# Kernel tuning notes

Hardware: AMD Instinct MI355X
Metric: run time of the kernel (lower is better)

The kernel has to match this reference:

```python
import jax, jax.numpy as jnp
from jax import lax
import numpy as np

B, T, D, H, K = 16, 1024, 1024, 1024, 2


def setup_inputs() -> dict:
    key = jax.random.key(0)
    k1, k2 = jax.random.split(key, 2)
    inputs = jax.random.normal(k1, (B, T, D), dtype=jnp.float32)
    # small init so tanh/sigmoid gates are not saturated
    conv_w = jax.random.normal(k2, (3 * H, D, K), dtype=jnp.float32) * 0.02
    conv_b = jnp.zeros((3 * H,), dtype=jnp.float32)
    return {"inputs": inputs, "conv_w": conv_w, "conv_b": conv_b, "layer_idx": 0}


def _qrnn_forward(inputs, conv_w, conv_b):
    k = conv_w.shape[-1]
    h = conv_w.shape[0] // 3
    # causal conv1d: pad (k-1) on the left of the time axis
    x = jnp.transpose(inputs, (0, 2, 1))                 # [B, D, T]
    x = jnp.pad(x, ((0, 0), (0, 0), (k - 1, 0)))         # [B, D, T+k-1]
    gates = lax.conv_general_dilated(
        x, conv_w, window_strides=(1,), padding="VALID",
        dimension_numbers=("NCH", "OIH", "NCH"))         # [B, 3H, T]
    gates = jnp.transpose(gates, (0, 2, 1)) + conv_b     # [B, T, 3H]
    Z = jnp.tanh(gates[..., :h])
    F = jax.nn.sigmoid(gates[..., h:2 * h])
    O = jax.nn.sigmoid(gates[..., 2 * h:])

    # fo-pooling recurrence: c_t = f_t * c_{t-1} + (1 - f_t) * z_t, c_0 = 0
    def step(c, zf):
        z, f = zf
        c_ = f * c + (1.0 - f) * z
        return c_, c_

    c0 = jnp.zeros((Z.shape[0], h), dtype=Z.dtype)
    zT = jnp.transpose(Z, (1, 0, 2))                     # [T, B, H]
    fT = jnp.transpose(F, (1, 0, 2))
    _, cT = lax.scan(step, c0, (zT, fT))                 # [T, B, H]
    c_time = jnp.transpose(cT, (1, 0, 2))                # [B, T, H]
    h_time = O * c_time
    return c_time, h_time


def reference(inputs, conv_w, conv_b, layer_idx):
    # layer_idx=0 with state=None, memory=None: no conv_linear memory term,
    # no attention, zero initial cell state.
    return _qrnn_forward(inputs, conv_w, conv_b)
```

## Files before the change

### kernel.cpp

```cpp
#include <hip/hip_runtime.h>

#define BB 16
#define TT 1024
#define DD 1024
#define HH 1024
#define NN 3072
#define KK 2048
#define MM (BB * TT)
#define TP (TT + 1)
#define NCH 32
#define TC  32

typedef __attribute__((ext_vector_type(8))) short short8;
typedef __attribute__((ext_vector_type(4))) float float4v;

__device__ __forceinline__ unsigned short f2bf(float f) {
    unsigned int u = __float_as_uint(f);
    u += 0x7fffu + ((u >> 16) & 1u);
    return (unsigned short)(u >> 16);
}
__device__ __forceinline__ float bf2f(unsigned short s) {
    return __uint_as_float(((unsigned int)s) << 16);
}

__device__ __forceinline__ void gload_lds16(const unsigned short* g, unsigned short* l) {
    __builtin_amdgcn_global_load_lds(
        (const __attribute__((address_space(1))) unsigned int*)(g),
        (__attribute__((address_space(3))) unsigned int*)(l),
        16, 0, 0);
}

__global__ __launch_bounds__(256) void pack_x_kernel(const float* __restrict__ x,
                                                     unsigned short* __restrict__ xpad) {
    int i = blockIdx.x * 256 + threadIdx.x;
    int total = BB * TP * (DD / 4);
    if (i >= total) return;
    int d4  = i & (DD / 4 - 1);
    int row = i >> 8;
    int b  = row / TP;
    int tp = row - b * TP;
    float4 v = make_float4(0.f, 0.f, 0.f, 0.f);
    if (tp > 0)
        v = ((const float4*)x)[(((size_t)(b * TT + tp - 1)) << 8) + d4];
    ushort4 r4;
    r4.x = f2bf(v.x); r4.y = f2bf(v.y); r4.z = f2bf(v.z); r4.w = f2bf(v.w);
    *(ushort4*)(xpad + (((size_t)row) << 10) + (d4 << 2)) = r4;
}

__global__ __launch_bounds__(256) void pack_w_kernel(const float* __restrict__ w,
                                                     unsigned short* __restrict__ Bt) {
    int i = blockIdx.x * 256 + threadIdx.x;
    if (i >= NN * DD) return;
    int n = i >> 10, d = i & 1023;
    float2 v = ((const float2*)w)[i];
    Bt[(size_t)n * KK + d]       = f2bf(v.x);
    Bt[(size_t)n * KK + DD + d]  = f2bf(v.y);
}

__global__ __launch_bounds__(256) void gemm_gates_kernel(const unsigned short* __restrict__ xpad,
                                                         const unsigned short* __restrict__ Bt,
                                                         const float* __restrict__ bias,
                                                         unsigned short* __restrict__ zfo) {
    __shared__ unsigned short As[128 * 32];
    __shared__ unsigned short Bs[128 * 32];

    const int tid  = threadIdx.x;
    const int lane = tid & 63;
    const int wave = tid >> 6;
    const int m0 = blockIdx.x * 128;
    const int n0 = blockIdx.y * 128;

    const int bidx = m0 >> 10;
    const int t0   = m0 & 1023;
    const unsigned short* aBase = xpad + (((size_t)(bidx * TP + t0)) << 10);

    const int msub = (wave & 1) << 6;
    const int nsub = (wave >> 1) << 6;
    const int mrow = lane & 15;
    const int quad = lane >> 4;
    const int csw = (quad ^ ((mrow >> 1) & 3)) << 3;

    float4v acc[4][4];
#pragma unroll
    for (int i = 0; i < 4; i++)
#pragma unroll
        for (int j = 0; j < 4; j++) acc[i][j] = (float4v)0.0f;

    for (int kb = 0; kb < KK / 32; ++kb) {
        const int tap = kb >> 5;
        const int kd0 = (kb & 31) << 5;
#pragma unroll
        for (int q = 0; q < 2; ++q) {
            int ci = q * 256 + tid;
            int r  = ci >> 2;
            int cs = (((ci & 3) ^ ((r >> 1) & 3)) << 3);
            gload_lds16(aBase + (((size_t)(r + tap)) << 10) + kd0 + cs, As + ci * 8);
            gload_lds16(Bt + (size_t)(n0 + r) * KK + (kb << 5) + cs, Bs + ci * 8);
        }
        __syncthreads();

        short8 af[4], bf[4];
#pragma unroll
        for (int i = 0; i < 4; i++) {
            af[i] = *(const short8*)(As + (msub + i * 16 + mrow) * 32 + csw);
            bf[i] = *(const short8*)(Bs + (nsub + i * 16 + mrow) * 32 + csw);
        }
#pragma unroll
        for (int i = 0; i < 4; i++)
#pragma unroll
            for (int j = 0; j < 4; j++)
                acc[i][j] = __builtin_amdgcn_mfma_f32_16x16x32_bf16(af[i], bf[j], acc[i][j], 0, 0, 0);
        __syncthreads();
    }

    const bool isZ = (n0 < HH);
#pragma unroll
    for (int j = 0; j < 4; j++) {
        int gcol = n0 + nsub + j * 16 + mrow;
        float bv = bias[gcol];
#pragma unroll
        for (int i = 0; i < 4; i++) {
            int mbase = m0 + msub + i * 16 + quad * 4;
#pragma unroll
            for (int r = 0; r < 4; r++) {
                float v = acc[i][j][r] + bv;
                float g;
                if (isZ) {
                    float s = __builtin_amdgcn_rcpf(1.0f + __expf(-2.0f * v));
                    g = 2.0f * s - 1.0f;
                } else {
                    g = __builtin_amdgcn_rcpf(1.0f + __expf(-v));
                }
                zfo[(size_t)(mbase + r) * NN + gcol] = f2bf(g);
            }
        }
    }
}


__global__ __launch_bounds__(256) void scan_summary_kernel(const unsigned short* __restrict__ zfo,
                                                           float2* __restrict__ P2,
                                                           float2* __restrict__ S2) {
    int g = blockIdx.x * 256 + threadIdx.x;
    int j = g >> 13;
    int b = (g >> 9) & 15;
    int h = (g & 511) << 1;
    const unsigned short* base = zfo + (size_t)b * TT * NN + h + (size_t)(j * TC) * NN;
    float c0 = 0.f, c1 = 0.f, p0 = 1.f, p1 = 1.f;
#pragma unroll 8
    for (int k = 0; k < TC; ++k) {
        const unsigned short* p = base + (size_t)k * NN;
        ushort2 z2 = *(const ushort2*)p;
        ushort2 f2 = *(const ushort2*)(p + HH);
        float z0 = bf2f(z2.x), z1 = bf2f(z2.y);
        float f0 = bf2f(f2.x), f1 = bf2f(f2.y);
        c0 = fmaf(f0, c0, (1.0f - f0) * z0);
        c1 = fmaf(f1, c1, (1.0f - f1) * z1);
        p0 *= f0;
        p1 *= f1;
    }
    P2[g] = make_float2(p0, p1);
    S2[g] = make_float2(c0, c1);
}

__global__ __launch_bounds__(256) void scan_prefix_kernel(const float* __restrict__ P,
                                                          const float* __restrict__ S,
                                                          float* __restrict__ Cin) {
    int idx = blockIdx.x * 256 + threadIdx.x;
    float c = 0.f;
#pragma unroll
    for (int j = 0; j < NCH; ++j) {
        int o = (j << 14) + idx;
        Cin[o] = c;
        c = fmaf(P[o], c, S[o]);
    }
}

__global__ __launch_bounds__(256) void scan_apply_kernel(const unsigned short* __restrict__ zfo,
                                                         const float2* __restrict__ Cin2,
                                                         float* __restrict__ out) {
    int g = blockIdx.x * 256 + threadIdx.x;
    int j = g >> 13;
    int b = (g >> 9) & 15;
    int h = (g & 511) << 1;
    const unsigned short* base = zfo + (size_t)b * TT * NN + h + (size_t)(j * TC) * NN;
    float* cp = out + (size_t)b * TT * HH + h + (size_t)(j * TC) * HH;
    float* hp = cp + (size_t)BB * TT * HH;
    float2 ci = Cin2[g];
    float c0 = ci.x, c1 = ci.y;
#pragma unroll 8
    for (int k = 0; k < TC; ++k) {
        const unsigned short* p = base + (size_t)k * NN;
        ushort2 z2 = *(const ushort2*)p;
        ushort2 f2 = *(const ushort2*)(p + HH);
        ushort2 o2 = *(const ushort2*)(p + 2 * HH);
        float z0 = bf2f(z2.x), z1 = bf2f(z2.y);
        float f0 = bf2f(f2.x), f1 = bf2f(f2.y);
        float o0 = bf2f(o2.x), o1 = bf2f(o2.y);
        c0 = fmaf(f0, c0, (1.0f - f0) * z0);
        c1 = fmaf(f1, c1, (1.0f - f1) * z1);
        *(float2*)(cp + (size_t)k * HH) = make_float2(c0, c1);
        *(float2*)(hp + (size_t)k * HH) = make_float2(o0 * c0, o1 * c1);
    }
}

extern "C" void kernel_launch(void* const* d_in, const int* in_sizes, int n_in,
                              void* d_out, int out_size, void* d_ws, size_t ws_size,
                              hipStream_t stream) {
    const float* x    = (const float*)d_in[0];
    const float* w    = (const float*)d_in[1];
    const float* bias = (const float*)d_in[2];
    float* out = (float*)d_out;

    char* ws = (char*)d_ws;
    const size_t xpad_bytes = (size_t)BB * TP * DD * 2;
    const size_t btw_bytes  = (size_t)NN * KK * 2;
    unsigned short* xpad = (unsigned short*)ws;
    unsigned short* Btw  = (unsigned short*)(ws + xpad_bytes);
    unsigned short* zfo  = (unsigned short*)(ws + xpad_bytes + btw_bytes);
    float* P   = (float*)ws;
    float* S   = (float*)(ws + (size_t)MM * NCH * 4);
    float* Cin = (float*)(ws + (size_t)MM * NCH * 8);

    {
        int total = BB * TP * (DD / 4);
        pack_x_kernel<<<(total + 255) / 256, 256, 0, stream>>>(x, xpad);
    }
    {
        int total = NN * DD;
        pack_w_kernel<<<(total + 255) / 256, 256, 0, stream>>>(w, Btw);
    }
    {
        dim3 grid(MM / 128, NN / 128);
        gemm_gates_kernel<<<grid, 256, 0, stream>>>(xpad, Btw, bias, zfo);
    }
    scan_summary_kernel<<<(MM / 2) * NCH / 256, 256, 0, stream>>>(zfo, (float2*)P, (float2*)S);
    scan_prefix_kernel<<<MM / 256, 256, 0, stream>>>(P, S, Cin);
    scan_apply_kernel<<<(MM / 2) * NCH / 256, 256, 0, stream>>>(zfo, (const float2*)Cin, out);
}
```

Before: 503.9 us.

## Store gate activations time-contiguous per gate plane via LDS transpose

The GEMM epilogue now stages activated gates in swizzled shared memory and writes them transposed into three separate planes (z, f, o), with time contiguous for each (batch, hidden) pair. The scan summary and apply kernels switch to one hidden unit per thread and read 32 timesteps with wide 16-byte vector loads instead of strided 4-byte loads. This targets the poorly coalesced reads in the scan phase. The trade-off is an extra LDS round trip and sync in the GEMM epilogue, and scan output stores become single floats strided by H across time.

```diff
diff --git a/kernel.cpp b/kernel.cpp
--- a/kernel.cpp
+++ b/kernel.cpp
@@ -10,6 +10,7 @@
 #define TP (TT + 1)
 #define NCH 32
 #define TC  32
+#define PLANE (1u << 24)
 
 typedef __attribute__((ext_vector_type(8))) short short8;
 typedef __attribute__((ext_vector_type(4))) float float4v;
@@ -60,9 +61,10 @@
 __global__ __launch_bounds__(256) void gemm_gates_kernel(const unsigned short* __restrict__ xpad,
                                                          const unsigned short* __restrict__ Bt,
                                                          const float* __restrict__ bias,
-                                                         unsigned short* __restrict__ zfo) {
-    __shared__ unsigned short As[128 * 32];
-    __shared__ unsigned short Bs[128 * 32];
+                                                         unsigned short* __restrict__ zT) {
+    __shared__ unsigned short smem[16384];
+    unsigned short* As = smem;
+    unsigned short* Bs = smem + 4096;
 
     const int tid  = threadIdx.x;
     const int lane = tid & 63;
@@ -112,55 +114,86 @@
                 acc[i][j] = __builtin_amdgcn_mfma_f32_16x16x32_bf16(af[i], bf[j], acc[i][j], 0, 0, 0);
         __syncthreads();
     }
+    unsigned short* Ts = smem;
 
     const bool isZ = (n0 < HH);
 #pragma unroll
     for (int j = 0; j < 4; j++) {
-        int gcol = n0 + nsub + j * 16 + mrow;
-        float bv = bias[gcol];
+        int nloc = nsub + j * 16 + mrow;
+        float bv = bias[n0 + nloc];
 #pragma unroll
         for (int i = 0; i < 4; i++) {
-            int mbase = m0 + msub + i * 16 + quad * 4;
-#pragma unroll
-            for (int r = 0; r < 4; r++) {
-                float v = acc[i][j][r] + bv;
-                float g;
+            int mcol = msub + i * 16 + (quad << 2);
+            unsigned int d0, d1;
+            {
+                float v0 = acc[i][j][0] + bv, v1 = acc[i][j][1] + bv;
+                float v2 = acc[i][j][2] + bv, v3 = acc[i][j][3] + bv;
+                float g0, g1, g2, g3;
                 if (isZ) {
-                    float s = __builtin_amdgcn_rcpf(1.0f + __expf(-2.0f * v));
-                    g = 2.0f * s - 1.0f;
+                    g0 = 2.0f * __builtin_amdgcn_rcpf(1.0f + __expf(-2.0f * v0)) - 1.0f;
+                    g1 = 2.0f * __builtin_amdgcn_rcpf(1.0f + __expf(-2.0f * v1)) - 1.0f;
+                    g2 = 2.0f * __builtin_amdgcn_rcpf(1.0f + __expf(-2.0f * v2)) - 1.0f;
+                    g3 = 2.0f * __builtin_amdgcn_rcpf(1.0f + __expf(-2.0f * v3)) - 1.0f;
                 } else {
-                    g = __builtin_amdgcn_rcpf(1.0f + __expf(-v));
+                    g0 = __builtin_amdgcn_rcpf(1.0f + __expf(-v0));
+                    g1 = __builtin_amdgcn_rcpf(1.0f + __expf(-v1));
+                    g2 = __builtin_amdgcn_rcpf(1.0f + __expf(-v2));
+                    g3 = __builtin_amdgcn_rcpf(1.0f + __expf(-v3));
                 }
-                zfo[(size_t)(mbase + r) * NN + gcol] = f2bf(g);
+                d0 = (unsigned int)f2bf(g0) | ((unsigned int)f2bf(g1) << 16);
+                d1 = (unsigned int)f2bf(g2) | ((unsigned int)f2bf(g3) << 16);
             }
-        }
-    }
-}
-
-
-__global__ __launch_bounds__(256) void scan_summary_kernel(const unsigned short* __restrict__ zfo,
-                                                           float2* __restrict__ P2,
-                                                           float2* __restrict__ S2) {
+            int chunk = (mcol >> 3) ^ (nloc & 7);
+            int el = nloc * 128 + (chunk << 3) + (mcol & 7);
+            *(uint2*)(Ts + el) = make_uint2(d0, d1);
+        }
+    }
+    __syncthreads();
+
+    const int rl = tid & 15;
+    const int rg = tid >> 4;
+    const int gate = n0 >> 10;
+    unsigned short* plane = zT + ((size_t)gate << 24);
+#pragma unroll
+    for (int p = 0; p < 8; p++) {
+        int np = (p << 4) + rg;
+        int lchunk = rl ^ (np & 7);
+        short8 vv = *(const short8*)(Ts + np * 128 + (lchunk << 3));
+        int h = (n0 & 1023) + np;
+        size_t dst = ((((size_t)((bidx << 10) | h)) << 10) | (unsigned)(t0 + (rl << 3)));
+        *(short8*)(plane + dst) = vv;
+    }
+}
+
+
+__global__ __launch_bounds__(256) void scan_summary_kernel(const unsigned short* __restrict__ zT,
+                                                           float* __restrict__ P,
+                                                           float* __restrict__ S) {
     int g = blockIdx.x * 256 + threadIdx.x;
-    int j = g >> 13;
-    int b = (g >> 9) & 15;
-    int h = (g & 511) << 1;
-    const unsigned short* base = zfo + (size_t)b * TT * NN + h + (size_t)(j * TC) * NN;
-    float c0 = 0.f, c1 = 0.f, p0 = 1.f, p1 = 1.f;
-#pragma unroll 8
-    for (int k = 0; k < TC; ++k) {
-        const unsigned short* p = base + (size_t)k * NN;
-        ushort2 z2 = *(const ushort2*)p;
-        ushort2 f2 = *(const ushort2*)(p + HH);
-        float z0 = bf2f(z2.x), z1 = bf2f(z2.y);
-        float f0 = bf2f(f2.x), f1 = bf2f(f2.y);
-        c0 = fmaf(f0, c0, (1.0f - f0) * z0);
-        c1 = fmaf(f1, c1, (1.0f - f1) * z1);
-        p0 *= f0;
-        p1 *= f1;
-    }
-    P2[g] = make_float2(p0, p1);
-    S2[g] = make_float2(c0, c1);
+    int h = g & 1023;
+    int b = (g >> 10) & 15;
+    int j = g >> 14;
+    const unsigned short* zp = zT + ((((size_t)((b << 10) | h)) << 10) + j * TC);
+    const unsigned short* fp = zp + PLANE;
+    short8 zv[4], fv[4];
+#pragma unroll
+    for (int q = 0; q < 4; ++q) {
+        zv[q] = *(const short8*)(zp + q * 8);
+        fv[q] = *(const short8*)(fp + q * 8);
+    }
+    float c = 0.f, pr = 1.f;
+#pragma unroll
+    for (int q = 0; q < 4; ++q)
+#pragma unroll
+        for (int k = 0; k < 8; ++k) {
+            float z = bf2f((unsigned short)zv[q][k]);
+            float f = bf2f((unsigned short)fv[q][k]);
+            c = fmaf(f, c, (1.0f - f) * z);
+            pr *= f;
+        }
+    int o = (j << 14) | (b << 10) | h;
+    P[o] = pr;
+    S[o] = c;
 }
 
 __global__ __launch_bounds__(256) void scan_prefix_kernel(const float* __restrict__ P,
@@ -176,32 +209,37 @@
     }
 }
 
-__global__ __launch_bounds__(256) void scan_apply_kernel(const unsigned short* __restrict__ zfo,
-                                                         const float2* __restrict__ Cin2,
+__global__ __launch_bounds__(256) void scan_apply_kernel(const unsigned short* __restrict__ zT,
+                                                         const float* __restrict__ Cin,
                                                          float* __restrict__ out) {
     int g = blockIdx.x * 256 + threadIdx.x;
-    int j = g >> 13;
-    int b = (g >> 9) & 15;
-    int h = (g & 511) << 1;
-    const unsigned short* base = zfo + (size_t)b * TT * NN + h + (size_t)(j * TC) * NN;
-    float* cp = out + (size_t)b * TT * HH + h + (size_t)(j * TC) * HH;
-    float* hp = cp + (size_t)BB * TT * HH;
-    float2 ci = Cin2[g];
-    float c0 = ci.x, c1 = ci.y;
-#pragma unroll 8
-    for (int k = 0; k < TC; ++k) {
-        const unsigned short* p = base + (size_t)k * NN;
-        ushort2 z2 = *(const ushort2*)p;
-        ushort2 f2 = *(const ushort2*)(p + HH);
-        ushort2 o2 = *(const ushort2*)(p + 2 * HH);
-        float z0 = bf2f(z2.x), z1 = bf2f(z2.y);
-        float f0 = bf2f(f2.x), f1 = bf2f(f2.y);
-        float o0 = bf2f(o2.x), o1 = bf2f(o2.y);
-        c0 = fmaf(f0, c0, (1.0f - f0) * z0);
-        c1 = fmaf(f1, c1, (1.0f - f1) * z1);
-        *(float2*)(cp + (size_t)k * HH) = make_float2(c0, c1);
-        *(float2*)(hp + (size_t)k * HH) = make_float2(o0 * c0, o1 * c1);
-    }
+    int h = g & 1023;
+    int b = (g >> 10) & 15;
+    int j = g >> 14;
+    const unsigned short* zp = zT + ((((size_t)((b << 10) | h)) << 10) + j * TC);
+    const unsigned short* fp = zp + PLANE;
+    const unsigned short* op = zp + 2 * (size_t)PLANE;
+    short8 zv[4], fv[4], ov[4];
+#pragma unroll
+    for (int q = 0; q < 4; ++q) {
+        zv[q] = *(const short8*)(zp + q * 8);
+        fv[q] = *(const short8*)(fp + q * 8);
+        ov[q] = *(const short8*)(op + q * 8);
+    }
+    float c = Cin[(j << 14) | (b << 10) | h];
+    float* cbase = out + ((((size_t)((b << 10) | (j * TC))) << 10) | h);
+#pragma unroll
+    for (int q = 0; q < 4; ++q)
+#pragma unroll
+        for (int k = 0; k < 8; ++k) {
+            float z = bf2f((unsigned short)zv[q][k]);
+            float f = bf2f((unsigned short)fv[q][k]);
+            float o = bf2f((unsigned short)ov[q][k]);
+            c = fmaf(f, c, (1.0f - f) * z);
+            float* cp = cbase + (((size_t)(q * 8 + k)) << 10);
+            cp[0] = c;
+            cp[(size_t)1 << 24] = o * c;
+        }
 }
 
 extern "C" void kernel_launch(void* const* d_in, const int* in_sizes, int n_in,
@@ -217,7 +255,7 @@
     const size_t btw_bytes  = (size_t)NN * KK * 2;
     unsigned short* xpad = (unsigned short*)ws;
     unsigned short* Btw  = (unsigned short*)(ws + xpad_bytes);
-    unsigned short* zfo  = (unsigned short*)(ws + xpad_bytes + btw_bytes);
+    unsigned short* zT   = (unsigned short*)(ws + xpad_bytes + btw_bytes);
     float* P   = (float*)ws;
     float* S   = (float*)(ws + (size_t)MM * NCH * 4);
     float* Cin = (float*)(ws + (size_t)MM * NCH * 8);
@@ -232,9 +270,9 @@
     }
     {
         dim3 grid(MM / 128, NN / 128);
-        gemm_gates_kernel<<<grid, 256, 0, stream>>>(xpad, Btw, bias, zfo);
-    }
-    scan_summary_kernel<<<(MM / 2) * NCH / 256, 256, 0, stream>>>(zfo, (float2*)P, (float2*)S);
+        gemm_gates_kernel<<<grid, 256, 0, stream>>>(xpad, Btw, bias, zT);
+    }
+    scan_summary_kernel<<<MM * NCH / 256, 256, 0, stream>>>(zT, P, S);
     scan_prefix_kernel<<<MM / 256, 256, 0, stream>>>(P, S, Cin);
-    scan_apply_kernel<<<(MM / 2) * NCH / 256, 256, 0, stream>>>(zfo, (const float2*)Cin, out);
-}
+    scan_apply_kernel<<<MM * NCH / 256, 256, 0, stream>>>(zT, Cin, out);
+}
```

Result: no change. 498.3 us (-1.1%).
